# Kernel tuning notes

Measured on AMD Instinct MI355X. Metric: run time of the kernel, lower is better.

The kernel has to match this reference:

```python
import jax, jax.numpy as jnp
import numpy as np

N_NODES = 100000
N_EDGES = 1600000
IN_CH = 128
HID = 128   # 2 * out_channels
OUT_CH = 64


def setup_inputs() -> dict:
    key = jax.random.key(0)
    k1, k2, k3, k4, k5, k6 = jax.random.split(key, 6)
    x = jax.random.normal(k1, (N_NODES, IN_CH), dtype=jnp.float32)
    edge_index = jax.random.randint(k2, (2, N_EDGES), 0, N_NODES, dtype=jnp.int64)
    W1 = jax.random.normal(k3, (IN_CH, HID), dtype=jnp.float32) / np.sqrt(IN_CH)
    b1 = jax.random.normal(k4, (HID,), dtype=jnp.float32) * 0.01
    W2 = jax.random.normal(k5, (HID, OUT_CH), dtype=jnp.float32) / np.sqrt(HID)
    b2 = jax.random.normal(k6, (OUT_CH,), dtype=jnp.float32) * 0.01
    return {"x": x, "edge_index": edge_index, "W1": W1, "b1": b1, "W2": W2, "b2": b2}


def _gcn_layer(x, src, dst, norm, W, b, n_nodes):
    # GCNConv: linear transform, then normalized scatter-add aggregation + bias
    h = x @ W                                   # [N, d_out]
    msg = h[src] * norm[:, None]                # gather + edge normalize, [E+N, d_out]
    out = jax.ops.segment_sum(msg, dst, num_segments=n_nodes)
    return out + b


def reference(x, edge_index, W1, b1, W2, b2):
    n = x.shape[0]
    loop = jnp.arange(n, dtype=edge_index.dtype)
    # add self-loops (PyG GCNConv default)
    src = jnp.concatenate([edge_index[0], loop])
    dst = jnp.concatenate([edge_index[1], loop])
    # symmetric normalization deg^-1/2[src] * deg^-1/2[dst]
    deg = jax.ops.segment_sum(jnp.ones_like(dst, x.dtype), dst, num_segments=n)
    dinv = jnp.where(deg > 0, jax.lax.rsqrt(deg), 0.0)
    norm = dinv[src] * dinv[dst]

    h = jax.nn.relu(_gcn_layer(x, src, dst, norm, W1, b1, n))
    out = jax.nn.relu(_gcn_layer(h, src, dst, norm, W2, b2, n))
    return out
```

## Files before the change

kernel.cpp:

```cpp
#include <hip/hip_runtime.h>
#include <hip/hip_fp16.h>

typedef _Float16 f16x8 __attribute__((ext_vector_type(8)));
typedef float f32x4 __attribute__((ext_vector_type(4)));

#define BSH 9
#define BSZ 512
#define CAP 12288

__global__ __launch_bounds__(256) void passA(const int* __restrict__ ei,
                                             int* __restrict__ bcount, int E, int NB) {
  __shared__ int hist[256];
  int t = threadIdx.x;
  hist[t] = 0;
  __syncthreads();
  for (int e = blockIdx.x * 256 + t; e < E; e += gridDim.x * 256)
    atomicAdd(&hist[ei[E + e] >> BSH], 1);
  __syncthreads();
  if (t < NB && hist[t]) atomicAdd(&bcount[t], hist[t]);
}

__global__ __launch_bounds__(256) void scanB(const int* __restrict__ bcount,
                                             int* __restrict__ bstart,
                                             int* __restrict__ bfill, int NB, int E) {
  __shared__ int s[256];
  int t = threadIdx.x;
  int v = (t < NB) ? bcount[t] : 0;
  s[t] = v;
  __syncthreads();
  for (int off = 1; off < 256; off <<= 1) {
    int add = (t >= off) ? s[t - off] : 0;
    __syncthreads();
    s[t] += add;
    __syncthreads();
  }
  if (t < NB) {
    int ex = s[t] - v;
    bstart[t] = ex;
    bfill[t] = ex;
  }
  if (t == 0) bstart[NB] = E;
}

template <int NC, int NWC, bool IN_F16, bool SCALE>
__device__ __forceinline__ void gemm_mfma_body(
    const void* __restrict__ Xv, const float* __restrict__ W,
    const float* __restrict__ dinv, _Float16* __restrict__ G, int nrows, int bid,
    _Float16* Bs) {
  int t = threadIdx.x;
  {
    int n = t % NC;
    int kh = (t / NC) * (NC / 2);
    constexpr int NBLK = (NC / 2) / 8;
#pragma unroll
    for (int b = 0; b < NBLK; ++b) {
      f16x8 tmp;
#pragma unroll
      for (int j = 0; j < 8; ++j)
        tmp[j] = (_Float16)W[(size_t)(kh + b * 8 + j) * NC + n];
      *(f16x8*)(&Bs[n * 136 + kh + b * 8]) = tmp;
    }
  }
  __syncthreads();

  int w = t >> 6, lane = t & 63;
  int m = lane & 15, q = lane >> 4;
  int wr = (w / NWC) * 64, wc = (w % NWC) * 64;
  int row0 = bid * ((4 / NWC) * 64);

  f32x4 acc[4][4];
#pragma unroll
  for (int rt = 0; rt < 4; ++rt)
#pragma unroll
    for (int ct = 0; ct < 4; ++ct)
#pragma unroll
      for (int qq = 0; qq < 4; ++qq) acc[rt][ct][qq] = 0.f;

#pragma unroll
  for (int kc = 0; kc < 4; ++kc) {
    int kbase = kc * 32 + q * 8;
    f16x8 af[4];
#pragma unroll
    for (int rt = 0; rt < 4; ++rt) {
      int row = row0 + wr + rt * 16 + m;
      if constexpr (IN_F16) {
        f16x8 a = {0, 0, 0, 0, 0, 0, 0, 0};
        if (row < nrows) a = *(const f16x8*)((const _Float16*)Xv + (size_t)row * 128 + kbase);
        af[rt] = a;
      } else {
        float4 x0 = {0, 0, 0, 0}, x1 = {0, 0, 0, 0};
        if (row < nrows) {
          const float* Xf = (const float*)Xv;
          x0 = *(const float4*)(Xf + (size_t)row * 128 + kbase);
          x1 = *(const float4*)(Xf + (size_t)row * 128 + kbase + 4);
        }
        f16x8 a;
        a[0] = (_Float16)x0.x; a[1] = (_Float16)x0.y;
        a[2] = (_Float16)x0.z; a[3] = (_Float16)x0.w;
        a[4] = (_Float16)x1.x; a[5] = (_Float16)x1.y;
        a[6] = (_Float16)x1.z; a[7] = (_Float16)x1.w;
        af[rt] = a;
      }
    }
    f16x8 bf[4];
#pragma unroll
    for (int ct = 0; ct < 4; ++ct) {
      int n = wc + ct * 16 + m;
      bf[ct] = *(f16x8*)(&Bs[n * 136 + kbase]);
    }
#pragma unroll
    for (int rt = 0; rt < 4; ++rt)
#pragma unroll
      for (int ct = 0; ct < 4; ++ct)
        acc[rt][ct] = __builtin_amdgcn_mfma_f32_16x16x32_f16(af[rt], bf[ct],
                                                             acc[rt][ct], 0, 0, 0);
  }
#pragma unroll
  for (int rt = 0; rt < 4; ++rt) {
#pragma unroll
    for (int r = 0; r < 4; ++r) {
      int row = row0 + wr + rt * 16 + q * 4 + r;
      if (row < nrows) {
        float d = SCALE ? dinv[row] : 1.f;
#pragma unroll
        for (int ct = 0; ct < 4; ++ct) {
          int col = wc + ct * 16 + m;
          G[(size_t)row * NC + col] = (_Float16)(acc[rt][ct][r] * d);
        }
      }
    }
  }
}

__global__ __launch_bounds__(256) void fused_gemm_passB(
    const float* __restrict__ X, const float* __restrict__ W1,
    _Float16* __restrict__ G, int nrows, int GB,
    const int* __restrict__ ei, int* __restrict__ bfill,
    unsigned int* __restrict__ pairs, int E, int PB) {
  __shared__ char smem[128 * 136 * 2];
  int g = blockIdx.x;
  int M2 = 2 * (GB < PB ? GB : PB);
  bool is_gemm;
  int bid;
  if (g < M2) { is_gemm = (g & 1) == 0; bid = g >> 1; }
  else        { is_gemm = (GB > PB);    bid = g - M2 + (GB < PB ? GB : PB); }
  if (is_gemm) {
    gemm_mfma_body<128, 2, false, false>(X, W1, nullptr, G, nrows, bid,
                                         (_Float16*)smem);
  } else {
    int* hist = (int*)smem;
    int* gbase = (int*)(smem + 1024);
    int t = threadIdx.x;
    hist[t] = 0;
    __syncthreads();
    int d[8], s[8], lp[8], bb[8];
    int base = bid * 2048;
#pragma unroll
    for (int u = 0; u < 8; ++u) {
      int e = base + u * 256 + t;
      if (e < E) {
        d[u] = ei[E + e];
        s[u] = ei[e];
        bb[u] = d[u] >> BSH;
        lp[u] = atomicAdd(&hist[bb[u]], 1);
      } else {
        bb[u] = -1;
      }
    }
    __syncthreads();
    if (hist[t]) gbase[t] = atomicAdd(&bfill[t], hist[t]);
    __syncthreads();
#pragma unroll
    for (int u = 0; u < 8; ++u)
      if (bb[u] >= 0)
        pairs[gbase[bb[u]] + lp[u]] =
            ((unsigned int)(d[u] & (BSZ - 1)) << 17) | (unsigned int)s[u];
  }
}

__global__ __launch_bounds__(256) void gemm2_mfma(const _Float16* __restrict__ X,
                                                  const float* __restrict__ W,
                                                  const float* __restrict__ dinv,
                                                  _Float16* __restrict__ G, int nrows) {
  __shared__ _Float16 Bs[64 * 136];
  gemm_mfma_body<64, 1, true, true>(X, W, dinv, G, nrows, blockIdx.x, Bs);
}

__global__ __launch_bounds__(512) void passC(const unsigned int* __restrict__ pairs,
                                             const int* __restrict__ bstart,
                                             int* __restrict__ rowstart,
                                             int* __restrict__ deg,
                                             float* __restrict__ dinv,
                                             int* __restrict__ csr, int N) {
  __shared__ int hcnt[BSZ];
  __shared__ int lfill[BSZ];
  __shared__ int ss[512];
  __shared__ int lcsr[CAP];
  int b = blockIdx.x;
  int t = threadIdx.x;
  int lo = bstart[b], hi = bstart[b + 1];
  int cnt = hi - lo;
  int nbase = b << BSH;
  hcnt[t] = 0;
  __syncthreads();
  for (int k = lo + t; k < hi; k += 512)
    atomicAdd(&hcnt[(pairs[k] >> 17) & (BSZ - 1)], 1);
  __syncthreads();
  int v = hcnt[t];
  ss[t] = v;
  __syncthreads();
  for (int off = 1; off < 512; off <<= 1) {
    int add = (t >= off) ? ss[t - off] : 0;
    __syncthreads();
    ss[t] += add;
    __syncthreads();
  }
  int ex = ss[t] - v;
  lfill[t] = ex;
  int node = nbase + t;
  if (node < N) {
    rowstart[node] = lo + ex;
    deg[node] = v;
    dinv[node] = rsqrtf((float)(v + 1));
  }
  __syncthreads();
  bool fits = (cnt <= CAP);
  for (int k = lo + t; k < hi; k += 512) {
    unsigned int p = pairs[k];
    int pos = atomicAdd(&lfill[(p >> 17) & (BSZ - 1)], 1);
    int src = (int)(p & 0x1FFFFu);
    if (fits) lcsr[pos] = src;
    else      csr[lo + pos] = src;
  }
  __syncthreads();
  if (fits)
    for (int k = t; k < cnt; k += 512) csr[lo + k] = lcsr[k];
}

__global__ __launch_bounds__(256) void agg128(
    const __half* __restrict__ G, const int* __restrict__ csr,
    const int* __restrict__ rowstart, const int* __restrict__ deg,
    const float* __restrict__ dinv, const float* __restrict__ bias,
    __half* __restrict__ out, int n) {
  int wid = blockIdx.x * 4 + (threadIdx.x >> 6);
  if (wid >= n) return;
  int i = __builtin_amdgcn_readfirstlane(wid);
  int lane = threadIdx.x & 63;
  const __half2* Gp = (const __half2*)G;
  float di = dinv[i];
  float2 g = __half22float2(Gp[(size_t)i * 64 + lane]);
  float2 a = {di * g.x, di * g.y};
  int s = rowstart[i];
  int d = deg[i];
  int cnt = d < 64 ? d : 64;
  int myidx = 0;
  if (lane < cnt) myidx = csr[s + lane];
  int k = 0;
  for (; k + 3 < cnt; k += 4) {
    int s0 = __builtin_amdgcn_readfirstlane(__shfl(myidx, k));
    int s1 = __builtin_amdgcn_readfirstlane(__shfl(myidx, k + 1));
    int s2 = __builtin_amdgcn_readfirstlane(__shfl(myidx, k + 2));
    int s3 = __builtin_amdgcn_readfirstlane(__shfl(myidx, k + 3));
    float w0 = dinv[s0], w1 = dinv[s1], w2 = dinv[s2], w3 = dinv[s3];
    float2 v0 = __half22float2(Gp[(size_t)s0 * 64 + lane]);
    float2 v1 = __half22float2(Gp[(size_t)s1 * 64 + lane]);
    float2 v2 = __half22float2(Gp[(size_t)s2 * 64 + lane]);
    float2 v3 = __half22float2(Gp[(size_t)s3 * 64 + lane]);
    a.x = fmaf(w0, v0.x, a.x); a.y = fmaf(w0, v0.y, a.y);
    a.x = fmaf(w1, v1.x, a.x); a.y = fmaf(w1, v1.y, a.y);
    a.x = fmaf(w2, v2.x, a.x); a.y = fmaf(w2, v2.y, a.y);
    a.x = fmaf(w3, v3.x, a.x); a.y = fmaf(w3, v3.y, a.y);
  }
  for (; k < cnt; ++k) {
    int s0 = __builtin_amdgcn_readfirstlane(__shfl(myidx, k));
    float w0 = dinv[s0];
    float2 v0 = __half22float2(Gp[(size_t)s0 * 64 + lane]);
    a.x = fmaf(w0, v0.x, a.x); a.y = fmaf(w0, v0.y, a.y);
  }
  for (int j = s + 64; j < s + d; ++j) {
    int s0 = __builtin_amdgcn_readfirstlane(csr[j]);
    float w0 = dinv[s0];
    float2 v0 = __half22float2(Gp[(size_t)s0 * 64 + lane]);
    a.x = fmaf(w0, v0.x, a.x); a.y = fmaf(w0, v0.y, a.y);
  }
  float2 b = ((const float2*)bias)[lane];
  float ox = fmaxf(fmaf(di, a.x, b.x), 0.f);
  float oy = fmaxf(fmaf(di, a.y, b.y), 0.f);
  ((__half2*)out)[(size_t)i * 64 + lane] = __floats2half2_rn(ox, oy);
}

__global__ __launch_bounds__(256) void agg64(
    const __half* __restrict__ G, const int* __restrict__ csr,
    const int* __restrict__ rowstart, const int* __restrict__ deg,
    const float* __restrict__ dinv, const float* __restrict__ bias,
    float* __restrict__ out, int n) {
  int wid = blockIdx.x * 4 + (threadIdx.x >> 6);
  if (wid >= n) return;
  int i = __builtin_amdgcn_readfirstlane(wid);
  int lane = threadIdx.x & 63;
  float a = __half2float(G[(size_t)i * 64 + lane]);
  int s = rowstart[i];
  int d = deg[i];
  int cnt = d < 64 ? d : 64;
  int myidx = 0;
  if (lane < cnt) myidx = csr[s + lane];
  int k = 0;
  for (; k + 3 < cnt; k += 4) {
    int s0 = __builtin_amdgcn_readfirstlane(__shfl(myidx, k));
    int s1 = __builtin_amdgcn_readfirstlane(__shfl(myidx, k + 1));
    int s2 = __builtin_amdgcn_readfirstlane(__shfl(myidx, k + 2));
    int s3 = __builtin_amdgcn_readfirstlane(__shfl(myidx, k + 3));
    float v0 = __half2float(G[(size_t)s0 * 64 + lane]);
    float v1 = __half2float(G[(size_t)s1 * 64 + lane]);
    float v2 = __half2float(G[(size_t)s2 * 64 + lane]);
    float v3 = __half2float(G[(size_t)s3 * 64 + lane]);
    a += (v0 + v1) + (v2 + v3);
  }
  for (; k < cnt; ++k) {
    int s0 = __builtin_amdgcn_readfirstlane(__shfl(myidx, k));
    a += __half2float(G[(size_t)s0 * 64 + lane]);
  }
  for (int j = s + 64; j < s + d; ++j) {
    int s0 = __builtin_amdgcn_readfirstlane(csr[j]);
    a += __half2float(G[(size_t)s0 * 64 + lane]);
  }
  float o = fmaxf(fmaf(dinv[i], a, bias[lane]), 0.f);
  out[(size_t)i * 64 + lane] = o;
}

extern "C" void kernel_launch(void* const* d_in, const int* in_sizes, int n_in,
                              void* d_out, int out_size, void* d_ws, size_t ws_size,
                              hipStream_t stream) {
  const float* x  = (const float*)d_in[0];
  const int*   ei = (const int*)d_in[1];
  const float* W1 = (const float*)d_in[2];
  const float* b1 = (const float*)d_in[3];
  const float* W2 = (const float*)d_in[4];
  const float* b2 = (const float*)d_in[5];
  float* out = (float*)d_out;

  const int N = in_sizes[0] / 128;
  const int E = in_sizes[1] / 2;
  const int NB = (N + BSZ - 1) >> BSH;

  char* base = (char*)d_ws;
  size_t off = 0;
  auto alloc = [&](size_t bytes) -> void* {
    void* p = base + off;
    off += (bytes + 255) & ~(size_t)255;
    return p;
  };
  int*          bcount   = (int*)alloc(256 * 4);
  int*          bstart   = (int*)alloc(260 * 4);
  int*          bfill    = (int*)alloc(256 * 4);
  int*          deg      = (int*)alloc((size_t)N * 4);
  int*          rowstart = (int*)alloc((size_t)N * 4);
  float*        dinv     = (float*)alloc((size_t)N * 4);
  int*          csr      = (int*)alloc((size_t)E * 4);
  unsigned int* pairs    = (unsigned int*)alloc((size_t)E * 4);
  __half*       g1       = (__half*)alloc((size_t)N * 128 * 2);
  __half*       x2       = (__half*)alloc((size_t)N * 128 * 2);

  hipMemsetAsync(bcount, 0, 256 * 4, stream);
  passA<<<512, 256, 0, stream>>>(ei, bcount, E, NB);
  scanB<<<1, 256, 0, stream>>>(bcount, bstart, bfill, NB, E);

  int GB = (N + 127) / 128;
  int PB = (E + 2047) / 2048;
  fused_gemm_passB<<<GB + PB, 256, 0, stream>>>(x, W1, (_Float16*)g1, N, GB, ei,
                                                bfill, pairs, E, PB);
  passC<<<NB, 512, 0, stream>>>(pairs, bstart, rowstart, deg, dinv, csr, N);

  agg128<<<(N + 3) / 4, 256, 0, stream>>>(g1, csr, rowstart, deg, dinv, b1, x2, N);
  int G2B = (N + 255) / 256;
  gemm2_mfma<<<G2B, 256, 0, stream>>>((const _Float16*)x2, W2, dinv,
                                      (_Float16*)g1, N);
  agg64<<<(N + 3) / 4, 256, 0, stream>>>(g1, csr, rowstart, deg, dinv, b2, out, N);
}
```

Baseline: 297.7 us.

## Fuse layer-1 aggregation with second GEMM in a persistent kernel

Merges the first-layer aggregation and the second GEMM into one persistent kernel. Each block caches W2 in shared memory as half2, and each wave multiplies its aggregated ReLU row by W2 in registers before writing only the 64-wide G2. This removes the 128-wide intermediate write and reread and one kernel launch, but the small GEMM now runs as scalar FMAs instead of MFMA. Both aggregation kernels also drop the lane-shuffle index prefetch and read CSR indices directly through uniform loads.

Measured after the change: 301.2 us. No clear change (+1.2%).

```diff
diff --git a/kernel.cpp b/kernel.cpp
--- a/kernel.cpp
+++ b/kernel.cpp
@@ -178,14 +178,6 @@
   }
 }
 
-__global__ __launch_bounds__(256) void gemm2_mfma(const _Float16* __restrict__ X,
-                                                  const float* __restrict__ W,
-                                                  const float* __restrict__ dinv,
-                                                  _Float16* __restrict__ G, int nrows) {
-  __shared__ _Float16 Bs[64 * 136];
-  gemm_mfma_body<64, 1, true, true>(X, W, dinv, G, nrows, blockIdx.x, Bs);
-}
-
 __global__ __launch_bounds__(512) void passC(const unsigned int* __restrict__ pairs,
                                              const int* __restrict__ bstart,
                                              int* __restrict__ rowstart,
@@ -237,56 +229,66 @@
     for (int k = t; k < cnt; k += 512) csr[lo + k] = lcsr[k];
 }
 
-__global__ __launch_bounds__(256) void agg128(
+__global__ __launch_bounds__(256) void agg128_g2(
     const __half* __restrict__ G, const int* __restrict__ csr,
     const int* __restrict__ rowstart, const int* __restrict__ deg,
-    const float* __restrict__ dinv, const float* __restrict__ bias,
-    __half* __restrict__ out, int n) {
-  int wid = blockIdx.x * 4 + (threadIdx.x >> 6);
-  if (wid >= n) return;
-  int i = __builtin_amdgcn_readfirstlane(wid);
-  int lane = threadIdx.x & 63;
+    const float* __restrict__ dinv, const float* __restrict__ b1,
+    const float* __restrict__ W2, __half* __restrict__ g2, int n, int ngroups) {
+  __shared__ __half2 W2s[64 * 64];
+  __shared__ float2 hbuf[4][64];
+  int t = threadIdx.x;
+  for (int idx = t; idx < 4096; idx += 256) {
+    int j = idx >> 6, c = idx & 63;
+    W2s[idx] = __floats2half2_rn(W2[(size_t)(2 * j) * 64 + c],
+                                 W2[(size_t)(2 * j + 1) * 64 + c]);
+  }
+  __syncthreads();
+
+  int w = t >> 6, lane = t & 63;
   const __half2* Gp = (const __half2*)G;
-  float di = dinv[i];
-  float2 g = __half22float2(Gp[(size_t)i * 64 + lane]);
-  float2 a = {di * g.x, di * g.y};
-  int s = rowstart[i];
-  int d = deg[i];
-  int cnt = d < 64 ? d : 64;
-  int myidx = 0;
-  if (lane < cnt) myidx = csr[s + lane];
-  int k = 0;
-  for (; k + 3 < cnt; k += 4) {
-    int s0 = __builtin_amdgcn_readfirstlane(__shfl(myidx, k));
-    int s1 = __builtin_amdgcn_readfirstlane(__shfl(myidx, k + 1));
-    int s2 = __builtin_amdgcn_readfirstlane(__shfl(myidx, k + 2));
-    int s3 = __builtin_amdgcn_readfirstlane(__shfl(myidx, k + 3));
-    float w0 = dinv[s0], w1 = dinv[s1], w2 = dinv[s2], w3 = dinv[s3];
-    float2 v0 = __half22float2(Gp[(size_t)s0 * 64 + lane]);
-    float2 v1 = __half22float2(Gp[(size_t)s1 * 64 + lane]);
-    float2 v2 = __half22float2(Gp[(size_t)s2 * 64 + lane]);
-    float2 v3 = __half22float2(Gp[(size_t)s3 * 64 + lane]);
-    a.x = fmaf(w0, v0.x, a.x); a.y = fmaf(w0, v0.y, a.y);
-    a.x = fmaf(w1, v1.x, a.x); a.y = fmaf(w1, v1.y, a.y);
-    a.x = fmaf(w2, v2.x, a.x); a.y = fmaf(w2, v2.y, a.y);
-    a.x = fmaf(w3, v3.x, a.x); a.y = fmaf(w3, v3.y, a.y);
-  }
-  for (; k < cnt; ++k) {
-    int s0 = __builtin_amdgcn_readfirstlane(__shfl(myidx, k));
-    float w0 = dinv[s0];
-    float2 v0 = __half22float2(Gp[(size_t)s0 * 64 + lane]);
-    a.x = fmaf(w0, v0.x, a.x); a.y = fmaf(w0, v0.y, a.y);
-  }
-  for (int j = s + 64; j < s + d; ++j) {
-    int s0 = __builtin_amdgcn_readfirstlane(csr[j]);
-    float w0 = dinv[s0];
-    float2 v0 = __half22float2(Gp[(size_t)s0 * 64 + lane]);
-    a.x = fmaf(w0, v0.x, a.x); a.y = fmaf(w0, v0.y, a.y);
-  }
-  float2 b = ((const float2*)bias)[lane];
-  float ox = fmaxf(fmaf(di, a.x, b.x), 0.f);
-  float oy = fmaxf(fmaf(di, a.y, b.y), 0.f);
-  ((__half2*)out)[(size_t)i * 64 + lane] = __floats2half2_rn(ox, oy);
+  for (int grp = blockIdx.x; grp < ngroups; grp += gridDim.x) {
+    int wid = grp * 4 + w;
+    if (wid < n) {
+      int i = __builtin_amdgcn_readfirstlane(wid);
+      float di = dinv[i];
+      float2 g = __half22float2(Gp[(size_t)i * 64 + lane]);
+      float2 a = {di * g.x, di * g.y};
+      int s = rowstart[i];
+      int d = deg[i];
+      int k = 0;
+      for (; k + 3 < d; k += 4) {
+        int s0 = csr[s + k], s1 = csr[s + k + 1];
+        int s2 = csr[s + k + 2], s3 = csr[s + k + 3];
+        float w0 = dinv[s0], w1 = dinv[s1], w2 = dinv[s2], w3 = dinv[s3];
+        float2 v0 = __half22float2(Gp[(size_t)s0 * 64 + lane]);
+        float2 v1 = __half22float2(Gp[(size_t)s1 * 64 + lane]);
+        float2 v2 = __half22float2(Gp[(size_t)s2 * 64 + lane]);
+        float2 v3 = __half22float2(Gp[(size_t)s3 * 64 + lane]);
+        a.x = fmaf(w0, v0.x, a.x); a.y = fmaf(w0, v0.y, a.y);
+        a.x = fmaf(w1, v1.x, a.x); a.y = fmaf(w1, v1.y, a.y);
+        a.x = fmaf(w2, v2.x, a.x); a.y = fmaf(w2, v2.y, a.y);
+        a.x = fmaf(w3, v3.x, a.x); a.y = fmaf(w3, v3.y, a.y);
+      }
+      for (; k < d; ++k) {
+        int s0 = csr[s + k];
+        float w0 = dinv[s0];
+        float2 v0 = __half22float2(Gp[(size_t)s0 * 64 + lane]);
+        a.x = fmaf(w0, v0.x, a.x); a.y = fmaf(w0, v0.y, a.y);
+      }
+      float2 b = ((const float2*)b1)[lane];
+      float hx = fmaxf(fmaf(di, a.x, b.x), 0.f);
+      float hy = fmaxf(fmaf(di, a.y, b.y), 0.f);
+      hbuf[w][lane] = make_float2(hx, hy);
+      float acc = 0.f;
+#pragma unroll 8
+      for (int j = 0; j < 64; ++j) {
+        float2 h = hbuf[w][j];
+        float2 wf = __half22float2(W2s[j * 64 + lane]);
+        acc = fmaf(h.x, wf.x, fmaf(h.y, wf.y, acc));
+      }
+      g2[(size_t)i * 64 + lane] = (__half)(acc * di);
+    }
+  }
 }
 
 __global__ __launch_bounds__(256) void agg64(
@@ -301,27 +303,18 @@
   float a = __half2float(G[(size_t)i * 64 + lane]);
   int s = rowstart[i];
   int d = deg[i];
-  int cnt = d < 64 ? d : 64;
-  int myidx = 0;
-  if (lane < cnt) myidx = csr[s + lane];
   int k = 0;
-  for (; k + 3 < cnt; k += 4) {
-    int s0 = __builtin_amdgcn_readfirstlane(__shfl(myidx, k));
-    int s1 = __builtin_amdgcn_readfirstlane(__shfl(myidx, k + 1));
-    int s2 = __builtin_amdgcn_readfirstlane(__shfl(myidx, k + 2));
-    int s3 = __builtin_amdgcn_readfirstlane(__shfl(myidx, k + 3));
+  for (; k + 3 < d; k += 4) {
+    int s0 = csr[s + k], s1 = csr[s + k + 1];
+    int s2 = csr[s + k + 2], s3 = csr[s + k + 3];
     float v0 = __half2float(G[(size_t)s0 * 64 + lane]);
     float v1 = __half2float(G[(size_t)s1 * 64 + lane]);
     float v2 = __half2float(G[(size_t)s2 * 64 + lane]);
     float v3 = __half2float(G[(size_t)s3 * 64 + lane]);
     a += (v0 + v1) + (v2 + v3);
   }
-  for (; k < cnt; ++k) {
-    int s0 = __builtin_amdgcn_readfirstlane(__shfl(myidx, k));
-    a += __half2float(G[(size_t)s0 * 64 + lane]);
-  }
-  for (int j = s + 64; j < s + d; ++j) {
-    int s0 = __builtin_amdgcn_readfirstlane(csr[j]);
+  for (; k < d; ++k) {
+    int s0 = csr[s + k];
     a += __half2float(G[(size_t)s0 * 64 + lane]);
   }
   float o = fmaxf(fmaf(dinv[i], a, bias[lane]), 0.f);
@@ -359,7 +352,7 @@
   int*          csr      = (int*)alloc((size_t)E * 4);
   unsigned int* pairs    = (unsigned int*)alloc((size_t)E * 4);
   __half*       g1       = (__half*)alloc((size_t)N * 128 * 2);
-  __half*       x2       = (__half*)alloc((size_t)N * 128 * 2);
+  __half*       g2       = (__half*)alloc((size_t)N * 64 * 2);
 
   hipMemsetAsync(bcount, 0, 256 * 4, stream);
   passA<<<512, 256, 0, stream>>>(ei, bcount, E, NB);
@@ -371,9 +364,8 @@
                                                 bfill, pairs, E, PB);
   passC<<<NB, 512, 0, stream>>>(pairs, bstart, rowstart, deg, dinv, csr, N);
 
-  agg128<<<(N + 3) / 4, 256, 0, stream>>>(g1, csr, rowstart, deg, dinv, b1, x2, N);
-  int G2B = (N + 255) / 256;
-  gemm2_mfma<<<G2B, 256, 0, stream>>>((const _Float16*)x2, W2, dinv,
-                                      (_Float16*)g1, N);
-  agg64<<<(N + 3) / 4, 256, 0, stream>>>(g1, csr, rowstart, deg, dinv, b2, out, N);
-}
+  int ngroups = (N + 3) / 4;
+  agg128_g2<<<2048, 256, 0, stream>>>(g1, csr, rowstart, deg, dinv, b1, W2, g2,
+                                      N, ngroups);
+  agg64<<<ngroups, 256, 0, stream>>>(g2, csr, rowstart, deg, dinv, b2, out, N);
+}
```

## Store features in 16-wide column slices and aggregate edges in parallel per wave

Applied to the files above, without the earlier changes.

The GEMM outputs and the layer-2 GEMM input switch from row-major to a sliced layout, [col/16][N][16] in fp16. The two aggregation kernels are rewritten to match: each block handles one 16-feature slice, and each wave gathers 8 neighbour edges at once with 8 lanes per edge, then reduces with xor-shuffles. The aim is to spread the slices across blocks and shrink each gather to a 32-byte segment to improve cache locality and parallelism. In exchange, the CSR index, degree and dinv loads are repeated once per slice, gathers become small 32-byte accesses, and layer 2 gets a separate g2 buffer.

After: 573.4 us. +92.6%, slower.

```diff
diff --git a/kernel.cpp b/kernel.cpp
--- a/kernel.cpp
+++ b/kernel.cpp
@@ -85,7 +85,10 @@
       int row = row0 + wr + rt * 16 + m;
       if constexpr (IN_F16) {
         f16x8 a = {0, 0, 0, 0, 0, 0, 0, 0};
-        if (row < nrows) a = *(const f16x8*)((const _Float16*)Xv + (size_t)row * 128 + kbase);
+        if (row < nrows)
+          a = *(const f16x8*)((const _Float16*)Xv +
+                              ((size_t)(kbase >> 4) * nrows + row) * 16 +
+                              (kbase & 15));
         af[rt] = a;
       } else {
         float4 x0 = {0, 0, 0, 0}, x1 = {0, 0, 0, 0};
@@ -125,7 +128,8 @@
 #pragma unroll
         for (int ct = 0; ct < 4; ++ct) {
           int col = wc + ct * 16 + m;
-          G[(size_t)row * NC + col] = (_Float16)(acc[rt][ct][r] * d);
+          G[((size_t)(col >> 4) * nrows + row) * 16 + (col & 15)] =
+              (_Float16)(acc[rt][ct][r] * d);
         }
       }
     }
@@ -237,95 +241,98 @@
     for (int k = t; k < cnt; k += 512) csr[lo + k] = lcsr[k];
 }
 
-__global__ __launch_bounds__(256) void agg128(
+__global__ __launch_bounds__(256) void agg128s(
     const __half* __restrict__ G, const int* __restrict__ csr,
     const int* __restrict__ rowstart, const int* __restrict__ deg,
-    const float* __restrict__ dinv, const float* __restrict__ bias,
-    __half* __restrict__ out, int n) {
-  int wid = blockIdx.x * 4 + (threadIdx.x >> 6);
-  if (wid >= n) return;
+    const float* __restrict__ dinv, const float* __restrict__ b1,
+    __half* __restrict__ x2, int N) {
+  int s = blockIdx.x & 7;
+  int grp = blockIdx.x >> 3;
+  int w = threadIdx.x >> 6, lane = threadIdx.x & 63;
+  int wid = grp * 4 + w;
+  if (wid >= N) return;
   int i = __builtin_amdgcn_readfirstlane(wid);
-  int lane = threadIdx.x & 63;
+  int e8 = lane >> 3, f = lane & 7;
   const __half2* Gp = (const __half2*)G;
+  size_t sbase = (size_t)s * N;
   float di = dinv[i];
-  float2 g = __half22float2(Gp[(size_t)i * 64 + lane]);
-  float2 a = {di * g.x, di * g.y};
-  int s = rowstart[i];
+  int r0 = rowstart[i];
   int d = deg[i];
-  int cnt = d < 64 ? d : 64;
-  int myidx = 0;
-  if (lane < cnt) myidx = csr[s + lane];
-  int k = 0;
-  for (; k + 3 < cnt; k += 4) {
-    int s0 = __builtin_amdgcn_readfirstlane(__shfl(myidx, k));
-    int s1 = __builtin_amdgcn_readfirstlane(__shfl(myidx, k + 1));
-    int s2 = __builtin_amdgcn_readfirstlane(__shfl(myidx, k + 2));
-    int s3 = __builtin_amdgcn_readfirstlane(__shfl(myidx, k + 3));
-    float w0 = dinv[s0], w1 = dinv[s1], w2 = dinv[s2], w3 = dinv[s3];
-    float2 v0 = __half22float2(Gp[(size_t)s0 * 64 + lane]);
-    float2 v1 = __half22float2(Gp[(size_t)s1 * 64 + lane]);
-    float2 v2 = __half22float2(Gp[(size_t)s2 * 64 + lane]);
-    float2 v3 = __half22float2(Gp[(size_t)s3 * 64 + lane]);
-    a.x = fmaf(w0, v0.x, a.x); a.y = fmaf(w0, v0.y, a.y);
-    a.x = fmaf(w1, v1.x, a.x); a.y = fmaf(w1, v1.y, a.y);
-    a.x = fmaf(w2, v2.x, a.x); a.y = fmaf(w2, v2.y, a.y);
-    a.x = fmaf(w3, v3.x, a.x); a.y = fmaf(w3, v3.y, a.y);
-  }
-  for (; k < cnt; ++k) {
-    int s0 = __builtin_amdgcn_readfirstlane(__shfl(myidx, k));
-    float w0 = dinv[s0];
-    float2 v0 = __half22float2(Gp[(size_t)s0 * 64 + lane]);
-    a.x = fmaf(w0, v0.x, a.x); a.y = fmaf(w0, v0.y, a.y);
-  }
-  for (int j = s + 64; j < s + d; ++j) {
-    int s0 = __builtin_amdgcn_readfirstlane(csr[j]);
-    float w0 = dinv[s0];
-    float2 v0 = __half22float2(Gp[(size_t)s0 * 64 + lane]);
-    a.x = fmaf(w0, v0.x, a.x); a.y = fmaf(w0, v0.y, a.y);
-  }
-  float2 b = ((const float2*)bias)[lane];
-  float ox = fmaxf(fmaf(di, a.x, b.x), 0.f);
-  float oy = fmaxf(fmaf(di, a.y, b.y), 0.f);
-  ((__half2*)out)[(size_t)i * 64 + lane] = __floats2half2_rn(ox, oy);
-}
-
-__global__ __launch_bounds__(256) void agg64(
-    const __half* __restrict__ G, const int* __restrict__ csr,
+  float2 acc = {0.f, 0.f};
+  for (int k = 0; k < d; k += 8) {
+    int ke = k + e8;
+    int idx = i;
+    float we = 0.f;
+    if (ke < d) {
+      idx = csr[r0 + ke];
+      we = dinv[idx];
+    }
+    float2 v = __half22float2(Gp[(sbase + idx) * 8 + f]);
+    acc.x = fmaf(we, v.x, acc.x);
+    acc.y = fmaf(we, v.y, acc.y);
+  }
+  acc.x += __shfl_xor(acc.x, 8);
+  acc.y += __shfl_xor(acc.y, 8);
+  acc.x += __shfl_xor(acc.x, 16);
+  acc.y += __shfl_xor(acc.y, 16);
+  acc.x += __shfl_xor(acc.x, 32);
+  acc.y += __shfl_xor(acc.y, 32);
+  if (e8 == 0) {
+    float2 g = __half22float2(Gp[(sbase + i) * 8 + f]);
+    float2 b = ((const float2*)b1)[s * 8 + f];
+    float hx = fmaxf(fmaf(di, fmaf(di, g.x, acc.x), b.x), 0.f);
+    float hy = fmaxf(fmaf(di, fmaf(di, g.y, acc.y), b.y), 0.f);
+    ((__half2*)x2)[(sbase + i) * 8 + f] = __floats2half2_rn(hx, hy);
+  }
+}
+
+__global__ __launch_bounds__(256) void agg64s(
+    const __half* __restrict__ G2, const int* __restrict__ csr,
     const int* __restrict__ rowstart, const int* __restrict__ deg,
-    const float* __restrict__ dinv, const float* __restrict__ bias,
-    float* __restrict__ out, int n) {
-  int wid = blockIdx.x * 4 + (threadIdx.x >> 6);
-  if (wid >= n) return;
+    const float* __restrict__ dinv, const float* __restrict__ b2,
+    float* __restrict__ out, int N, int Nh) {
+  int xs = blockIdx.x & 7;
+  int s = xs & 3, half = xs >> 2;
+  int grp = blockIdx.x >> 3;
+  int w = threadIdx.x >> 6, lane = threadIdx.x & 63;
+  int local = grp * 4 + w;
+  if (local >= Nh) return;
+  int wid = half * Nh + local;
+  if (wid >= N) return;
   int i = __builtin_amdgcn_readfirstlane(wid);
-  int lane = threadIdx.x & 63;
-  float a = __half2float(G[(size_t)i * 64 + lane]);
-  int s = rowstart[i];
+  int e8 = lane >> 3, f = lane & 7;
+  const __half2* Gp = (const __half2*)G2;
+  size_t sbase = (size_t)s * N;
+  int r0 = rowstart[i];
   int d = deg[i];
-  int cnt = d < 64 ? d : 64;
-  int myidx = 0;
-  if (lane < cnt) myidx = csr[s + lane];
-  int k = 0;
-  for (; k + 3 < cnt; k += 4) {
-    int s0 = __builtin_amdgcn_readfirstlane(__shfl(myidx, k));
-    int s1 = __builtin_amdgcn_readfirstlane(__shfl(myidx, k + 1));
-    int s2 = __builtin_amdgcn_readfirstlane(__shfl(myidx, k + 2));
-    int s3 = __builtin_amdgcn_readfirstlane(__shfl(myidx, k + 3));
-    float v0 = __half2float(G[(size_t)s0 * 64 + lane]);
-    float v1 = __half2float(G[(size_t)s1 * 64 + lane]);
-    float v2 = __half2float(G[(size_t)s2 * 64 + lane]);
-    float v3 = __half2float(G[(size_t)s3 * 64 + lane]);
-    a += (v0 + v1) + (v2 + v3);
-  }
-  for (; k < cnt; ++k) {
-    int s0 = __builtin_amdgcn_readfirstlane(__shfl(myidx, k));
-    a += __half2float(G[(size_t)s0 * 64 + lane]);
-  }
-  for (int j = s + 64; j < s + d; ++j) {
-    int s0 = __builtin_amdgcn_readfirstlane(csr[j]);
-    a += __half2float(G[(size_t)s0 * 64 + lane]);
-  }
-  float o = fmaxf(fmaf(dinv[i], a, bias[lane]), 0.f);
-  out[(size_t)i * 64 + lane] = o;
+  float2 acc = {0.f, 0.f};
+  for (int k = 0; k < d; k += 8) {
+    int ke = k + e8;
+    int idx = i;
+    float we = 0.f;
+    if (ke < d) {
+      idx = csr[r0 + ke];
+      we = 1.f;
+    }
+    float2 v = __half22float2(Gp[(sbase + idx) * 8 + f]);
+    acc.x = fmaf(we, v.x, acc.x);
+    acc.y = fmaf(we, v.y, acc.y);
+  }
+  acc.x += __shfl_xor(acc.x, 8);
+  acc.y += __shfl_xor(acc.y, 8);
+  acc.x += __shfl_xor(acc.x, 16);
+  acc.y += __shfl_xor(acc.y, 16);
+  acc.x += __shfl_xor(acc.x, 32);
+  acc.y += __shfl_xor(acc.y, 32);
+  if (e8 == 0) {
+    float di = dinv[i];
+    float2 g = __half22float2(Gp[(sbase + i) * 8 + f]);
+    float2 b = ((const float2*)b2)[s * 8 + f];
+    float2 o;
+    o.x = fmaxf(fmaf(di, g.x + acc.x, b.x), 0.f);
+    o.y = fmaxf(fmaf(di, g.y + acc.y, b.y), 0.f);
+    ((float2*)out)[(size_t)i * 32 + s * 8 + f] = o;
+  }
 }
 
 extern "C" void kernel_launch(void* const* d_in, const int* in_sizes, int n_in,
@@ -360,6 +367,7 @@
   unsigned int* pairs    = (unsigned int*)alloc((size_t)E * 4);
   __half*       g1       = (__half*)alloc((size_t)N * 128 * 2);
   __half*       x2       = (__half*)alloc((size_t)N * 128 * 2);
+  __half*       g2       = (__half*)alloc((size_t)N * 64 * 2);
 
   hipMemsetAsync(bcount, 0, 256 * 4, stream);
   passA<<<512, 256, 0, stream>>>(ei, bcount, E, NB);
@@ -371,9 +379,14 @@
                                                 bfill, pairs, E, PB);
   passC<<<NB, 512, 0, stream>>>(pairs, bstart, rowstart, deg, dinv, csr, N);
 
-  agg128<<<(N + 3) / 4, 256, 0, stream>>>(g1, csr, rowstart, deg, dinv, b1, x2, N);
+  int ng = (N + 3) / 4;
+  agg128s<<<8 * ng, 256, 0, stream>>>(g1, csr, rowstart, deg, dinv, b1, x2, N);
+
   int G2B = (N + 255) / 256;
   gemm2_mfma<<<G2B, 256, 0, stream>>>((const _Float16*)x2, W2, dinv,
-                                      (_Float16*)g1, N);
-  agg64<<<(N + 3) / 4, 256, 0, stream>>>(g1, csr, rowstart, deg, dinv, b2, out, N);
-}
+                                      (_Float16*)g2, N);
+
+  int Nh = (N + 1) / 2;
+  int ngh = (Nh + 3) / 4;
+  agg64s<<<8 * ngh, 256, 0, stream>>>(g2, csr, rowstart, deg, dinv, b2, out, N, Nh);
+}
```
